# Performance work log

Hardware: AMD Instinct MI355X
Metric: run time of the kernel (lower is better)

The kernel has to match this reference:

```python
import jax, jax.numpy as jnp
import numpy as np

N = 100000      # num_nodes
R = 8           # num_relations
D = 128         # hidden_dim
E = 600000      # num_edges
P = 100000      # num query pairs
PH = 128        # pair_hidden_dim


def _xavier(key, shape):
    fan_in, fan_out = shape[-2], shape[-1]
    limit = float(np.sqrt(6.0 / (fan_in + fan_out)))
    return jax.random.uniform(key, shape, jnp.float32, -limit, limit)


def setup_inputs() -> dict:
    key = jax.random.key(0)
    ks = jax.random.split(key, 16)
    edge_index = jax.random.randint(ks[0], (2, E), 0, N)
    edge_type = jax.random.randint(ks[1], (E,), 0, R)
    drug_index = jax.random.randint(ks[2], (P,), 0, N)
    disease_index = jax.random.randint(ks[3], (P,), 0, N)
    emb = _xavier(ks[4], (N, D))
    rw1 = _xavier(ks[5], (R, D, D))
    sl1 = _xavier(ks[6], (D, D))
    b1 = jnp.zeros((D,), jnp.float32)
    rw2 = _xavier(ks[7], (R, D, D))
    sl2 = _xavier(ks[8], (D, D))
    b2 = jnp.zeros((D,), jnp.float32)
    pw1 = _xavier(ks[9], (3 * D, PH))
    pb1 = jnp.zeros((PH,), jnp.float32)
    pw2 = _xavier(ks[10], (PH, 1))
    pb2 = jnp.zeros((1,), jnp.float32)
    return {
        "edge_index": edge_index, "edge_type": edge_type,
        "drug_index": drug_index, "disease_index": disease_index,
        "emb": emb, "rw1": rw1, "sl1": sl1, "b1": b1,
        "rw2": rw2, "sl2": sl2, "b2": b2,
        "pw1": pw1, "pb1": pb1, "pw2": pw2, "pb2": pb2,
    }


def _rgcn_layer(x, rel_w, self_w, bias, src, dst, etype):
    # Transform all node features once per relation: [R, N, D]
    xW = jnp.einsum('nd,rde->rne', x, rel_w)
    # Per-relation in-degree of dst (matches torch bincount-per-relation, clamp_min(1))
    seg_key = etype * N + dst                                  # [E]
    deg = jax.ops.segment_sum(jnp.ones((src.shape[0],), x.dtype), seg_key,
                              num_segments=R * N)
    deg = jnp.maximum(deg, 1.0)
    msg = xW[etype, src] / deg[seg_key][:, None]               # [E, D]
    agg = jax.ops.segment_sum(msg, dst, num_segments=N)        # [N, D]
    return x @ self_w + agg + bias


def reference(edge_index, edge_type, drug_index, disease_index,
              emb, rw1, sl1, b1, rw2, sl2, b2, pw1, pb1, pw2, pb2):
    src, dst = edge_index[0], edge_index[1]
    # encode (eval mode: dropout is identity)
    x = _rgcn_layer(emb, rw1, sl1, b1, src, dst, edge_type)
    x = jax.nn.relu(x)
    x = _rgcn_layer(x, rw2, sl2, b2, src, dst, edge_type)
    # score_pairs
    dh = x[drug_index]
    sh = x[disease_index]
    feat = jnp.concatenate((dh, sh, dh * sh), axis=-1)         # [P, 3D]
    h = jax.nn.relu(feat @ pw1 + pb1)
    logits = (h @ pw2 + pb2)[:, 0]                             # [P]
    return logits
```

## Files before the change

### kernel.cpp

```cpp
#include <hip/hip_runtime.h>

#define D 128

typedef short s16x8 __attribute__((ext_vector_type(8)));
typedef float f32x4 __attribute__((ext_vector_type(4)));

__device__ inline unsigned short f2b(float f) {
    unsigned u = __builtin_bit_cast(unsigned, f);
    unsigned r = (u + 0x7FFFu + ((u >> 16) & 1u)) >> 16;
    return (unsigned short)r;
}
__device__ inline float b2f(unsigned short h) {
    unsigned u = ((unsigned)h) << 16;
    return __builtin_bit_cast(float, u);
}


__global__ void k_count2(const int* __restrict__ etype, const int* __restrict__ dstA,
                         int E, int N, int* __restrict__ deg) {
    int e = blockIdx.x * blockDim.x + threadIdx.x;
    if (e < E) atomicAdd(&deg[etype[e] * N + dstA[e]], 1);
}


template<int VPT>
__global__ void k_scan_blk(const int* __restrict__ in, int* __restrict__ tmp,
                           int* __restrict__ bsum, int n) {
    __shared__ int sd[256];
    int t = threadIdx.x;
    long base = (long)blockIdx.x * (256 * VPT) + (long)t * VPT;
    int s[VPT];
    int tsum = 0;
    #pragma unroll
    for (int k = 0; k < VPT; ++k) { s[k] = (base + k < n) ? in[base + k] : 0; tsum += s[k]; }
    sd[t] = tsum;
    __syncthreads();
    for (int off = 1; off < 256; off <<= 1) {
        int v = (t >= off) ? sd[t - off] : 0;
        __syncthreads();
        sd[t] += v;
        __syncthreads();
    }
    int run = sd[t] - tsum;
    #pragma unroll
    for (int k = 0; k < VPT; ++k) { if (base + k < n) tmp[base + k] = run; run += s[k]; }
    if (t == 255) bsum[blockIdx.x] = sd[255];
}

__global__ void k_scan2(const int* __restrict__ bsum, int* __restrict__ boff, int nb) {
    __shared__ int sd[256];
    int t = threadIdx.x;
    int v = (t < nb) ? bsum[t] : 0;
    sd[t] = v;
    __syncthreads();
    for (int off = 1; off < 256; off <<= 1) {
        int w = (t >= off) ? sd[t - off] : 0;
        __syncthreads();
        sd[t] += w;
        __syncthreads();
    }
    if (t < nb) boff[t] = sd[t] - v;
}

__global__ void k_scan3(const int* __restrict__ tmp, const int* __restrict__ boff,
                        int* __restrict__ out, int n, int shift) {
    int i = blockIdx.x * 256 + threadIdx.x;
    if (i < n) out[i] = tmp[i] + boff[i >> shift];
}


__global__ void k_scatter(const int* __restrict__ etype, const int* __restrict__ srcA,
                          const int* __restrict__ dstA, int E, int N,
                          const int* __restrict__ degOff, int* __restrict__ binCur,
                          int* __restrict__ slotSrc) {
    int e = blockIdx.x * 256 + threadIdx.x;
    if (e < E) {
        int bin = etype[e] * N + dstA[e];
        int rank = atomicAdd(&binCur[bin], 1);
        slotSrc[degOff[bin] + rank] = srcA[e];
    }
}


__global__ void k_prep(const float* __restrict__ emb,
                       const float* __restrict__ rw1, const float* __restrict__ sl1,
                       const float* __restrict__ rw2, const float* __restrict__ sl2,
                       const float* __restrict__ pw1,
                       unsigned short* __restrict__ embb,
                       unsigned short* __restrict__ wAll1,
                       unsigned short* __restrict__ wAll2,
                       unsigned short* __restrict__ pw1T,
                       int N, int R)
{
    long t = (long)blockIdx.x * 256 + threadIdx.x;
    long u0 = (long)N * D / 4;
    if (t < u0) {
        long i = t * 4;
        f32x4 v = *(const f32x4*)(emb + i);
        unsigned a0 = (unsigned)f2b(v[0]) | ((unsigned)f2b(v[1]) << 16);
        unsigned a1 = (unsigned)f2b(v[2]) | ((unsigned)f2b(v[3]) << 16);
        uint2 o; o.x = a0; o.y = a1;
        *(uint2*)(embb + i) = o;
        return;
    }
    t -= u0;
    long uW = (long)(R + 1) * D * D;
    if (t < 2 * uW) {
        const float* rw = (t < uW) ? rw1 : rw2;
        const float* sl = (t < uW) ? sl1 : sl2;
        unsigned short* o = (t < uW) ? wAll1 : wAll2;
        long u = (t < uW) ? t : t - uW;
        int r = (int)(u >> 14);
        int nb = (int)(u & 16383);
        int n = nb >> 7, kk = nb & 127;
        int ke = kk ^ ((n & 7) << 3);
        float v = (r < R) ? rw[((size_t)r * D + ke) * D + n] : sl[(size_t)ke * D + n];
        o[u] = f2b(v);
        return;
    }
    t -= 2 * uW;
    if (t < 3 * D * D) {
        int n = (int)(t / 384), ck = (int)(t - n * 384);
        int ch = ck >> 7, kl = (ck & 127) ^ ((n & 7) << 3);
        pw1T[t] = f2b(pw1[(size_t)(ch * 128 + kl) * 128 + n]);
    }
}


template<bool RELU>
__global__ __launch_bounds__(256) void k_fused(
    const unsigned short* __restrict__ xb,
    const unsigned short* __restrict__ wAll,
    const int* __restrict__ slotSrc,
    const int* __restrict__ degOff,
    const float* __restrict__ bias,
    unsigned short* __restrict__ out,
    int N, int R, int E)
{
    __shared__ unsigned char smB[32768];
    __shared__ unsigned char smM[32768];
    int tid = threadIdx.x;
    int d0 = blockIdx.x * 128;
    int dmax = (d0 + 128 < N) ? d0 + 128 : N;

    int lane = tid & 63, wid = tid >> 6;
    int lo = lane & 15, hi = lane >> 4;
    int m = tid >> 1, ch = tid & 1;
    int dmine = d0 + m;

    float a[64];
    #pragma unroll
    for (int j = 0; j < 64; ++j) a[j] = 0.0f;

    for (int r = 0; r <= R; ++r) {
        int s0, cnt;
        if (r < R) {
            s0 = degOff[r * N + d0];
            int b1 = r * N + dmax;
            int s1 = (b1 < R * N) ? degOff[b1] : E;
            cnt = s1 - s0;
            if (cnt == 0) continue;
        } else {
            s0 = 0;
            cnt = dmax - d0;
        }

        {
            const int4* src = (const int4*)(wAll + (size_t)r * D * D);
            int4* dstl = (int4*)smB;
            #pragma unroll
            for (int i = 0; i < 8; ++i) dstl[tid + i * 256] = src[tid + i * 256];
        }
        __syncthreads();

        for (int c0 = 0; c0 < cnt; c0 += 128) {
            int i0 = c0 + wid * 32 + lo;
            int i1 = i0 + 16;
            int ci0 = (i0 < cnt) ? i0 : cnt - 1;
            int ci1 = (i1 < cnt) ? i1 : cnt - 1;
            int sv0, sv1;
            if (r < R) { sv0 = slotSrc[s0 + ci0]; sv1 = slotSrc[s0 + ci1]; }
            else       { sv0 = d0 + ci0;          sv1 = d0 + ci1; }
            const unsigned short* xr0 = xb + (size_t)sv0 * D;
            const unsigned short* xr1 = xb + (size_t)sv1 * D;
            s16x8 af0[4], af1[4];
            #pragma unroll
            for (int ks = 0; ks < 4; ++ks) {
                af0[ks] = *(const s16x8*)(xr0 + ks * 32 + hi * 8);
                af1[ks] = *(const s16x8*)(xr1 + ks * 32 + hi * 8);
            }

            f32x4 acc[2][8];
            #pragma unroll
            for (int q = 0; q < 2; ++q)
                #pragma unroll
                for (int n = 0; n < 8; ++n) acc[q][n] = (f32x4){0, 0, 0, 0};

            #pragma unroll
            for (int ks = 0; ks < 4; ++ks) {
                int kb = ks * 64 + hi * 16;
                #pragma unroll
                for (int n = 0; n < 8; ++n) {
                    int cr = n * 16 + lo;
                    s16x8 bf = *(const s16x8*)(smB + cr * 256 + (kb ^ ((cr & 7) << 4)));
                    acc[0][n] = __builtin_amdgcn_mfma_f32_16x16x32_bf16(af0[ks], bf, acc[0][n], 0, 0, 0);
                    acc[1][n] = __builtin_amdgcn_mfma_f32_16x16x32_bf16(af1[ks], bf, acc[1][n], 0, 0, 0);
                }
            }

            __syncthreads();
            #pragma unroll
            for (int m2 = 0; m2 < 2; ++m2) {
                int rbase = wid * 32 + m2 * 16 + hi * 4;
                #pragma unroll
                for (int reg = 0; reg < 4; ++reg) {
                    int rl = rbase + reg;
                    #pragma unroll
                    for (int n = 0; n < 8; ++n) {
                        int byteoff = rl * 256 + (((n * 32 + (lo >> 3) * 16) ^ ((rl & 7) << 4)) + (lo & 7) * 2);
                        *(unsigned short*)(smM + byteoff) = f2b(acc[m2][n][reg]);
                    }
                }
            }
            __syncthreads();

            if (dmine < N) {
                int st, en; float inv;
                if (r < R) {
                    int bin = r * N + dmine;
                    st = degOff[bin];
                    en = (bin + 1 < R * N) ? degOff[bin + 1] : E;
                    inv = (en > st) ? 1.0f / (float)(en - st) : 0.0f;
                } else {
                    st = m; en = m + 1; inv = 1.0f;
                }
                int loI = st > s0 + c0 ? st : s0 + c0;
                int hiI = en < s0 + c0 + 128 ? en : s0 + c0 + 128;
                for (int slot = loI; slot < hiI; ++slot) {
                    int rl = slot - (s0 + c0);
                    #pragma unroll
                    for (int g = 0; g < 8; ++g) {
                        int c = ch * 8 + g;
                        int4 v = *(const int4*)(smM + rl * 256 + ((c * 16) ^ ((rl & 7) << 4)));
                        const unsigned short* hp = (const unsigned short*)&v;
                        #pragma unroll
                        for (int k = 0; k < 8; ++k)
                            a[g * 8 + k] = fmaf(b2f(hp[k]), inv, a[g * 8 + k]);
                    }
                }
            }
            __syncthreads();
        }
    }

    if (dmine < N) {
        #pragma unroll
        for (int g = 0; g < 8; ++g) {
            unsigned short o8[8];
            #pragma unroll
            for (int k = 0; k < 8; ++k) {
                float v = a[g * 8 + k] + bias[ch * 64 + g * 8 + k];
                if (RELU) v = fmaxf(v, 0.0f);
                o8[k] = f2b(v);
            }
            *(int4*)(out + (size_t)dmine * D + ch * 64 + g * 8) = *(const int4*)o8;
        }
    }
}


__global__ __launch_bounds__(256) void k_score(
    const unsigned short* __restrict__ x2b,
    const int* __restrict__ drug, const int* __restrict__ dis,
    const unsigned short* __restrict__ pw1T,
    const float* __restrict__ pb1, const float* __restrict__ pw2,
    const float* __restrict__ pb2, float* __restrict__ outp, int P)
{
    __shared__ unsigned char smA[32768];
    __shared__ unsigned char smB[32768];
    __shared__ float pb1s[128];
    __shared__ float pw2s[128];
    int tid = threadIdx.x;
    long p0 = (long)blockIdx.x * 128;
    if (tid < 128) { pb1s[tid] = pb1[tid]; pw2s[tid] = pw2[tid]; }
    float pb2v = pb2[0];

    int lane = tid & 63, wid = tid >> 6;
    int lo = lane & 15, hi = lane >> 4;
    f32x4 acc[2][8];
    #pragma unroll
    for (int q = 0; q < 2; ++q)
        #pragma unroll
        for (int b = 0; b < 8; ++b) acc[q][b] = (f32x4){0, 0, 0, 0};

    for (int chn = 0; chn < 3; ++chn) {
        {
            const int4* src = (const int4*)pw1T;
            int4* dstl = (int4*)smB;
            #pragma unroll
            for (int i = 0; i < 8; ++i) {
                int q = tid + i * 256;
                int n = q >> 4, c = q & 15;
                dstl[q] = src[n * 48 + chn * 16 + c];
            }
        }
        {
            int m = tid >> 1, half = tid & 1;
            long p = p0 + m;
            int4 z = {0, 0, 0, 0};
            if (p < P) {
                const int4* da = (const int4*)(x2b + (size_t)drug[p] * D);
                const int4* db = (const int4*)(x2b + (size_t)dis[p] * D);
                for (int c = half * 8; c < half * 8 + 8; ++c) {
                    int4 v;
                    if (chn == 0) v = da[c];
                    else if (chn == 1) v = db[c];
                    else {
                        int4 va = da[c], vb = db[c];
                        const unsigned short* ap = (const unsigned short*)&va;
                        const unsigned short* bp = (const unsigned short*)&vb;
                        unsigned short o[8];
                        #pragma unroll
                        for (int j = 0; j < 8; ++j) o[j] = f2b(b2f(ap[j]) * b2f(bp[j]));
                        v = *(const int4*)o;
                    }
                    *(int4*)(smA + m * 256 + ((c * 16) ^ ((m & 7) << 4))) = v;
                }
            } else {
                for (int c = half * 8; c < half * 8 + 8; ++c)
                    *(int4*)(smA + m * 256 + ((c * 16) ^ ((m & 7) << 4))) = z;
            }
        }
        __syncthreads();

        #pragma unroll
        for (int ks = 0; ks < 4; ++ks) {
            int kb = ks * 64 + hi * 16;
            int r0 = wid * 32 + lo, r1 = r0 + 16;
            s16x8 a0 = *(const s16x8*)(smA + r0 * 256 + (kb ^ ((r0 & 7) << 4)));
            s16x8 a1 = *(const s16x8*)(smA + r1 * 256 + (kb ^ ((r1 & 7) << 4)));
            #pragma unroll
            for (int n = 0; n < 8; ++n) {
                int cr = n * 16 + lo;
                s16x8 bf = *(const s16x8*)(smB + cr * 256 + (kb ^ ((cr & 7) << 4)));
                acc[0][n] = __builtin_amdgcn_mfma_f32_16x16x32_bf16(a0, bf, acc[0][n], 0, 0, 0);
                acc[1][n] = __builtin_amdgcn_mfma_f32_16x16x32_bf16(a1, bf, acc[1][n], 0, 0, 0);
            }
        }
        __syncthreads();
    }

    #pragma unroll
    for (int m2 = 0; m2 < 2; ++m2)
        #pragma unroll
        for (int reg = 0; reg < 4; ++reg) {
            float s = 0.0f;
            #pragma unroll
            for (int n = 0; n < 8; ++n) {
                int col = n * 16 + lo;
                float v = acc[m2][n][reg] + pb1s[col];
                v = fmaxf(v, 0.0f);
                s = fmaf(v, pw2s[col], s);
            }
            s += __shfl_xor(s, 1, 64);
            s += __shfl_xor(s, 2, 64);
            s += __shfl_xor(s, 4, 64);
            s += __shfl_xor(s, 8, 64);
            long p = p0 + wid * 32 + m2 * 16 + hi * 4 + reg;
            if (lo == 0 && p < P) outp[p] = s + pb2v;
        }
}


extern "C" void kernel_launch(void* const* d_in, const int* in_sizes, int n_in,
                              void* d_out, int out_size, void* d_ws, size_t ws_size,
                              hipStream_t stream) {
    const int*   edge_index = (const int*)d_in[0];
    const int*   edge_type  = (const int*)d_in[1];
    const int*   drug       = (const int*)d_in[2];
    const int*   dis        = (const int*)d_in[3];
    const float* emb        = (const float*)d_in[4];
    const float* rw1        = (const float*)d_in[5];
    const float* sl1        = (const float*)d_in[6];
    const float* b1         = (const float*)d_in[7];
    const float* rw2        = (const float*)d_in[8];
    const float* sl2        = (const float*)d_in[9];
    const float* b2         = (const float*)d_in[10];
    const float* pw1        = (const float*)d_in[11];
    const float* pb1        = (const float*)d_in[12];
    const float* pw2        = (const float*)d_in[13];
    const float* pb2        = (const float*)d_in[14];

    const int E = in_sizes[1];
    const int P = in_sizes[2];
    const int N = in_sizes[4] / D;
    const int R = in_sizes[5] / (D * D);

    const int* srcA = edge_index;
    const int* dstA = edge_index + E;

    char* ws = (char*)d_ws;
    unsigned short* embb = (unsigned short*)ws; ws += (size_t)N * D * 2;
    unsigned short* x1b  = (unsigned short*)ws; ws += (size_t)N * D * 2;
    unsigned short* wAll1 = (unsigned short*)ws; ws += (size_t)(R + 1) * D * D * 2;
    unsigned short* wAll2 = (unsigned short*)ws; ws += (size_t)(R + 1) * D * D * 2;
    unsigned short* pw1T  = (unsigned short*)ws; ws += (size_t)3 * D * D * 2;
    int* deg     = (int*)ws; ws += (size_t)R * N * 4;
    int* binCur  = (int*)ws; ws += (size_t)R * N * 4;
    size_t zbytes = (size_t)(2 * R * N) * 4;
    int* slotSrc = (int*)ws; ws += (size_t)E * 4;
    int* degOff  = (int*)ws; ws += (size_t)R * N * 4;
    int* bsum    = (int*)ws; ws += 256 * 4;
    int* boff    = (int*)ws; ws += 256 * 4;
    unsigned short* x2b = embb;

    hipMemsetAsync(deg, 0, zbytes, stream);

    long u0 = (long)N * D / 4;
    long uW = (long)(R + 1) * D * D;
    long utot = u0 + 2 * uW + 3 * D * D;
    k_prep<<<(int)((utot + 255) / 256), 256, 0, stream>>>(emb, rw1, sl1, rw2, sl2, pw1,
                                                          embb, wAll1, wAll2, pw1T, N, R);

    k_count2<<<(E + 255) / 256, 256, 0, stream>>>(edge_type, dstA, E, N, deg);

    int nbS = (R * N + 4095) / 4096;
    k_scan_blk<16><<<nbS, 256, 0, stream>>>(deg, degOff, bsum, R * N);
    k_scan2<<<1, 256, 0, stream>>>(bsum, boff, nbS);
    k_scan3<<<(R * N + 255) / 256, 256, 0, stream>>>(degOff, boff, degOff, R * N, 12);

    k_scatter<<<(E + 255) / 256, 256, 0, stream>>>(edge_type, srcA, dstA, E, N,
                                                   degOff, binCur, slotSrc);

    int gridF = (N + 127) / 128;

    k_fused<true><<<gridF, 256, 0, stream>>>(embb, wAll1, slotSrc, degOff, b1, x1b, N, R, E);
    k_fused<false><<<gridF, 256, 0, stream>>>(x1b, wAll2, slotSrc, degOff, b2, x2b, N, R, E);

    k_score<<<(P + 127) / 128, 256, 0, stream>>>(x2b, drug, dis, pw1T, pb1, pw2, pb2,
                                                 (float*)d_out, P);
}
```

Measured before the change: 520.6 us.

## Aggregate neighbor features before relation matmul instead of transforming per edge

Reorders the RGCN layer so each destination node first gathers and mean-averages its neighbors' input features per relation, then multiplies the 128-row aggregated tile by the relation weight with MFMA. Previously every edge message was transformed individually and scattered back through shared memory. The change cuts the MFMA work from per-edge to per-node-per-relation, and the accumulator now lives in the MFMA registers across relations. B fragments are read straight from global memory, unswizzled, instead of being staged in LDS. The gather loop is a serial per-thread loop over each node's edges, which can be load-imbalanced and latency-bound, and rounding the averaged features to bf16 changes numerics slightly.

```diff
diff --git a/kernel.cpp b/kernel.cpp
--- a/kernel.cpp
+++ b/kernel.cpp
@@ -113,8 +113,7 @@
         int r = (int)(u >> 14);
         int nb = (int)(u & 16383);
         int n = nb >> 7, kk = nb & 127;
-        int ke = kk ^ ((n & 7) << 3);
-        float v = (r < R) ? rw[((size_t)r * D + ke) * D + n] : sl[(size_t)ke * D + n];
+        float v = (r < R) ? rw[((size_t)r * D + kk) * D + n] : sl[(size_t)kk * D + n];
         o[u] = f2b(v);
         return;
     }
@@ -137,133 +136,137 @@
     unsigned short* __restrict__ out,
     int N, int R, int E)
 {
-    __shared__ unsigned char smB[32768];
-    __shared__ unsigned char smM[32768];
+    __shared__ unsigned char smA[32768];
     int tid = threadIdx.x;
     int d0 = blockIdx.x * 128;
-    int dmax = (d0 + 128 < N) ? d0 + 128 : N;
-
+    int dmaxc = (d0 + 128 < N) ? d0 + 128 : N;
     int lane = tid & 63, wid = tid >> 6;
     int lo = lane & 15, hi = lane >> 4;
-    int m = tid >> 1, ch = tid & 1;
-    int dmine = d0 + m;
-
-    float a[64];
-    #pragma unroll
-    for (int j = 0; j < 64; ++j) a[j] = 0.0f;
+    int am = tid >> 2, ac = tid & 3;
+
+    f32x4 acc[2][8];
+    #pragma unroll
+    for (int q = 0; q < 2; ++q)
+        #pragma unroll
+        for (int n = 0; n < 8; ++n) acc[q][n] = (f32x4){0, 0, 0, 0};
 
     for (int r = 0; r <= R; ++r) {
-        int s0, cnt;
         if (r < R) {
-            s0 = degOff[r * N + d0];
-            int b1 = r * N + dmax;
-            int s1 = (b1 < R * N) ? degOff[b1] : E;
-            cnt = s1 - s0;
+            int b0 = r * N + d0;
+            int b1 = r * N + dmaxc;
+            int cnt = ((b1 < R * N) ? degOff[b1] : E) - degOff[b0];
             if (cnt == 0) continue;
-        } else {
-            s0 = 0;
-            cnt = dmax - d0;
-        }
+        }
+
+        #pragma unroll
+        for (int hf = 0; hf < 2; ++hf) {
+            int row = hf * 64 + am;
+            int d = d0 + row;
+            unsigned char* db = smA + row * 256;
+            int sw = (row & 7) << 4;
+            if (r == R) {
+                int4 v[4] = {{0,0,0,0},{0,0,0,0},{0,0,0,0},{0,0,0,0}};
+                if (d < N) {
+                    #pragma unroll
+                    for (int g = 0; g < 4; ++g)
+                        v[g] = *(const int4*)(xb + (size_t)d * D + (ac + 4 * g) * 8);
+                }
+                #pragma unroll
+                for (int g = 0; g < 4; ++g)
+                    *(int4*)(db + (((ac + 4 * g) * 16) ^ sw)) = v[g];
+            } else {
+                int st = 0, en = 0;
+                if (d < N) {
+                    int bin = r * N + d;
+                    st = degOff[bin];
+                    en = (bin + 1 < R * N) ? degOff[bin + 1] : E;
+                }
+                if (en > st) {
+                    float s[32];
+                    #pragma unroll
+                    for (int j = 0; j < 32; ++j) s[j] = 0.0f;
+                    for (int e2 = st; e2 < en; ++e2) {
+                        int src = slotSrc[e2];
+                        const unsigned short* xr = xb + (size_t)src * D;
+                        #pragma unroll
+                        for (int g = 0; g < 4; ++g) {
+                            int4 w = *(const int4*)(xr + (ac + 4 * g) * 8);
+                            const unsigned short* hp = (const unsigned short*)&w;
+                            #pragma unroll
+                            for (int k = 0; k < 8; ++k) s[g * 8 + k] += b2f(hp[k]);
+                        }
+                    }
+                    float inv = 1.0f / (float)(en - st);
+                    #pragma unroll
+                    for (int g = 0; g < 4; ++g) {
+                        unsigned short o8[8];
+                        #pragma unroll
+                        for (int k = 0; k < 8; ++k) o8[k] = f2b(s[g * 8 + k] * inv);
+                        *(int4*)(db + (((ac + 4 * g) * 16) ^ sw)) = *(const int4*)o8;
+                    }
+                } else {
+                    int4 z = {0, 0, 0, 0};
+                    #pragma unroll
+                    for (int g = 0; g < 4; ++g)
+                        *(int4*)(db + (((ac + 4 * g) * 16) ^ sw)) = z;
+                }
+            }
+        }
+        __syncthreads();
 
         {
-            const int4* src = (const int4*)(wAll + (size_t)r * D * D);
-            int4* dstl = (int4*)smB;
-            #pragma unroll
-            for (int i = 0; i < 8; ++i) dstl[tid + i * 256] = src[tid + i * 256];
-        }
-        __syncthreads();
-
-        for (int c0 = 0; c0 < cnt; c0 += 128) {
-            int i0 = c0 + wid * 32 + lo;
-            int i1 = i0 + 16;
-            int ci0 = (i0 < cnt) ? i0 : cnt - 1;
-            int ci1 = (i1 < cnt) ? i1 : cnt - 1;
-            int sv0, sv1;
-            if (r < R) { sv0 = slotSrc[s0 + ci0]; sv1 = slotSrc[s0 + ci1]; }
-            else       { sv0 = d0 + ci0;          sv1 = d0 + ci1; }
-            const unsigned short* xr0 = xb + (size_t)sv0 * D;
-            const unsigned short* xr1 = xb + (size_t)sv1 * D;
-            s16x8 af0[4], af1[4];
-            #pragma unroll
-            for (int ks = 0; ks < 4; ++ks) {
-                af0[ks] = *(const s16x8*)(xr0 + ks * 32 + hi * 8);
-                af1[ks] = *(const s16x8*)(xr1 + ks * 32 + hi * 8);
-            }
-
-            f32x4 acc[2][8];
-            #pragma unroll
-            for (int q = 0; q < 2; ++q)
-                #pragma unroll
-                for (int n = 0; n < 8; ++n) acc[q][n] = (f32x4){0, 0, 0, 0};
-
+            int r0g = wid * 32 + lo, r1g = r0g + 16;
+            s16x8 a0[4], a1[4];
             #pragma unroll
             for (int ks = 0; ks < 4; ++ks) {
                 int kb = ks * 64 + hi * 16;
+                a0[ks] = *(const s16x8*)(smA + r0g * 256 + (kb ^ ((r0g & 7) << 4)));
+                a1[ks] = *(const s16x8*)(smA + r1g * 256 + (kb ^ ((r1g & 7) << 4)));
+            }
+            const unsigned short* Bp = wAll + (size_t)r * D * D;
+            #pragma unroll
+            for (int ks = 0; ks < 4; ++ks) {
                 #pragma unroll
                 for (int n = 0; n < 8; ++n) {
-                    int cr = n * 16 + lo;
-                    s16x8 bf = *(const s16x8*)(smB + cr * 256 + (kb ^ ((cr & 7) << 4)));
-                    acc[0][n] = __builtin_amdgcn_mfma_f32_16x16x32_bf16(af0[ks], bf, acc[0][n], 0, 0, 0);
-                    acc[1][n] = __builtin_amdgcn_mfma_f32_16x16x32_bf16(af1[ks], bf, acc[1][n], 0, 0, 0);
+                    s16x8 bf = *(const s16x8*)(Bp + (size_t)(n * 16 + lo) * D + ks * 32 + hi * 8);
+                    acc[0][n] = __builtin_amdgcn_mfma_f32_16x16x32_bf16(a0[ks], bf, acc[0][n], 0, 0, 0);
+                    acc[1][n] = __builtin_amdgcn_mfma_f32_16x16x32_bf16(a1[ks], bf, acc[1][n], 0, 0, 0);
                 }
             }
-
-            __syncthreads();
-            #pragma unroll
-            for (int m2 = 0; m2 < 2; ++m2) {
-                int rbase = wid * 32 + m2 * 16 + hi * 4;
-                #pragma unroll
-                for (int reg = 0; reg < 4; ++reg) {
-                    int rl = rbase + reg;
-                    #pragma unroll
-                    for (int n = 0; n < 8; ++n) {
-                        int byteoff = rl * 256 + (((n * 32 + (lo >> 3) * 16) ^ ((rl & 7) << 4)) + (lo & 7) * 2);
-                        *(unsigned short*)(smM + byteoff) = f2b(acc[m2][n][reg]);
-                    }
-                }
-            }
-            __syncthreads();
-
-            if (dmine < N) {
-                int st, en; float inv;
-                if (r < R) {
-                    int bin = r * N + dmine;
-                    st = degOff[bin];
-                    en = (bin + 1 < R * N) ? degOff[bin + 1] : E;
-                    inv = (en > st) ? 1.0f / (float)(en - st) : 0.0f;
-                } else {
-                    st = m; en = m + 1; inv = 1.0f;
-                }
-                int loI = st > s0 + c0 ? st : s0 + c0;
-                int hiI = en < s0 + c0 + 128 ? en : s0 + c0 + 128;
-                for (int slot = loI; slot < hiI; ++slot) {
-                    int rl = slot - (s0 + c0);
-                    #pragma unroll
-                    for (int g = 0; g < 8; ++g) {
-                        int c = ch * 8 + g;
-                        int4 v = *(const int4*)(smM + rl * 256 + ((c * 16) ^ ((rl & 7) << 4)));
-                        const unsigned short* hp = (const unsigned short*)&v;
-                        #pragma unroll
-                        for (int k = 0; k < 8; ++k)
-                            a[g * 8 + k] = fmaf(b2f(hp[k]), inv, a[g * 8 + k]);
-                    }
-                }
-            }
-            __syncthreads();
-        }
-    }
-
-    if (dmine < N) {
-        #pragma unroll
-        for (int g = 0; g < 8; ++g) {
-            unsigned short o8[8];
-            #pragma unroll
-            for (int k = 0; k < 8; ++k) {
-                float v = a[g * 8 + k] + bias[ch * 64 + g * 8 + k];
+        }
+        __syncthreads();
+    }
+
+    float bb[8];
+    #pragma unroll
+    for (int n = 0; n < 8; ++n) bb[n] = bias[n * 16 + lo];
+    #pragma unroll
+    for (int m2 = 0; m2 < 2; ++m2) {
+        int rbase = wid * 32 + m2 * 16 + hi * 4;
+        #pragma unroll
+        for (int reg = 0; reg < 4; ++reg) {
+            int rl = rbase + reg;
+            #pragma unroll
+            for (int n = 0; n < 8; ++n) {
+                float v = acc[m2][n][reg] + bb[n];
                 if (RELU) v = fmaxf(v, 0.0f);
-                o8[k] = f2b(v);
-            }
-            *(int4*)(out + (size_t)dmine * D + ch * 64 + g * 8) = *(const int4*)o8;
+                int byteoff = rl * 256 + (((n * 32 + (lo >> 3) * 16) ^ ((rl & 7) << 4)) + (lo & 7) * 2);
+                *(unsigned short*)(smA + byteoff) = f2b(v);
+            }
+        }
+    }
+    __syncthreads();
+    {
+        int m = tid >> 1, chh = tid & 1;
+        int d = d0 + m;
+        if (d < N) {
+            unsigned short* op = out + (size_t)d * D;
+            #pragma unroll
+            for (int i = 0; i < 8; ++i) {
+                int c = chh * 8 + i;
+                int4 v = *(const int4*)(smA + m * 256 + ((c * 16) ^ ((m & 7) << 4)));
+                *(int4*)(op + c * 8) = v;
+            }
         }
     }
 }
```

After: 588.1 us. 1.13x slower.
